# Optimization experiments

Measured on AMD Instinct MI355X. Metric: run time of the kernel, lower is better.

The kernel has to match this reference:

```python
import jax, jax.numpy as jnp
import numpy as np

EXP_CLAMP = 1.0e6
DENOM_EPS = 1e-10
LRELU_ALPHA = 0.01


def setup_inputs() -> dict:
    key = jax.random.key(0)
    k1, k2, k3, k4, k5, k6 = jax.random.split(key, 6)
    B, N, E, F = 4, 16384, 262144, 64
    h = jax.random.normal(k1, (B, N, F), dtype=jnp.float32)
    edge = jax.random.randint(k2, (B, E, 2), 0, N, dtype=jnp.int32)
    edge_num = jax.random.randint(k3, (B,), 1, E, dtype=jnp.int32)
    edge_weight = jax.random.uniform(k4, (B, E), dtype=jnp.float32)
    W = jax.random.normal(k5, (F, F), dtype=jnp.float32) * 0.15  # xavier-ish scale
    a = jax.random.normal(k6, (1, 2 * F), dtype=jnp.float32) * 0.12
    return {"h": h, "edge": edge, "edge_num": edge_num,
            "edge_weight": edge_weight, "W": W, "a": a}


def _seg_sum(src, idx, num_segments):
    # src: [E, ...], idx: [E] -> [num_segments, ...]
    return jax.ops.segment_sum(src, idx, num_segments=num_segments)


def reference(h, edge, edge_num, edge_weight, W, a):
    B, N, Fin = h.shape
    E = edge.shape[1]
    # linear transform: Wh = h @ W^T  -> [B, N, Fout]
    Wh = jnp.einsum('bnf,of->bno', h, W)
    ctr = edge[:, :, 0]  # [B, E]
    nbr = edge[:, :, 1]  # [B, E]
    Wh_c = jnp.take_along_axis(Wh, ctr[:, :, None], axis=1)  # [B, E, Fout]
    Wh_n = jnp.take_along_axis(Wh, nbr[:, :, None], axis=1)  # [B, E, Fout]
    a_input = jnp.concatenate([Wh_c, Wh_n], axis=-1) * edge_weight[:, :, None]
    # attention logits: leakyrelu(a_input @ a^T), squeeze to [B, E]
    att1 = jax.nn.leaky_relu(jnp.einsum('bek,k->be', a_input, a[0]), LRELU_ALPHA)
    # per-batch valid-edge mask (edges beyond edge_num zeroed, as in torch loop)
    mask = (jnp.arange(E, dtype=jnp.int32)[None, :] < edge_num[:, None])
    x_exp = jnp.clip(jnp.exp(att1), 0.0, EXP_CLAMP) * mask.astype(att1.dtype)
    # segment softmax denominator over center nodes
    denom = DENOM_EPS + jax.vmap(_seg_sum, in_axes=(0, 0, None))(x_exp, ctr, N)  # [B, N]
    att = x_exp / jnp.take_along_axis(denom, ctr, axis=1)  # [B, E]
    # weighted neighbor aggregation via scatter-add on center index
    att_Wh = Wh_n * att[:, :, None]  # masked edges already have att == 0
    h_prime = jax.vmap(_seg_sum, in_axes=(0, 0, None))(att_Wh, ctr, N)  # [B, N, Fout]
    return jax.nn.relu(h_prime)
```

## Files before the change

### kernel.cpp

```cpp
#include <hip/hip_runtime.h>

#define BB 4
#define NN 16384
#define EE 262144
#define FF 64
#define ROWS (BB * NN)
#define CAP 64

typedef __bf16 bf16x8 __attribute__((ext_vector_type(8)));
typedef float  f32x4  __attribute__((ext_vector_type(4)));

__device__ __forceinline__ unsigned short f32_to_bf16(float f) {
    unsigned int u = __float_as_uint(f);
    u += 0x7FFFu + ((u >> 16) & 1u);
    return (unsigned short)(u >> 16);
}

__global__ __launch_bounds__(256) void scsn_kernel(
    const float* __restrict__ h, const float* __restrict__ W,
    const float* __restrict__ a,
    float* __restrict__ sc, float* __restrict__ sn, int* __restrict__ cnt)
{
    __shared__ float wc[FF], wn[FF];
    const int t = threadIdx.x;

    if (blockIdx.x < 256) cnt[blockIdx.x * 256 + t] = 0;

    if (t < 128) {
        const int f = t & 63;
        const float* av = a + (t >> 6) * FF;
        float s = 0.0f;
        #pragma unroll 8
        for (int o = 0; o < FF; ++o)
            s = fmaf(av[o], W[o * FF + f], s);
        (t < 64 ? wc : wn)[f] = s;
    }
    __syncthreads();

    const int gl   = t & 15;
    const int rloc = t >> 4;
    const float4 wcv = *(const float4*)&wc[gl * 4];
    const float4 wnv = *(const float4*)&wn[gl * 4];

    for (int base = blockIdx.x * 16; base < ROWS; base += gridDim.x * 16) {
        const int row = base + rloc;
        const float4 hv = ((const float4*)h)[(size_t)row * 16 + gl];
        float s1 = hv.x * wcv.x + hv.y * wcv.y + hv.z * wcv.z + hv.w * wcv.w;
        float s2 = hv.x * wnv.x + hv.y * wnv.y + hv.z * wnv.z + hv.w * wnv.w;
        #pragma unroll
        for (int off = 8; off; off >>= 1) {
            s1 += __shfl_xor(s1, off);
            s2 += __shfl_xor(s2, off);
        }
        if (gl == 0) { sc[row] = s1; sn[row] = s2; }
    }
}

__global__ __launch_bounds__(256) void mfma_bin_kernel(
    const float* __restrict__ h, const float* __restrict__ W,
    const int* __restrict__ edge, const int* __restrict__ edge_num,
    const float* __restrict__ ew,
    const float* __restrict__ sc, const float* __restrict__ sn,
    unsigned short* __restrict__ Wh, int* __restrict__ cnt,
    unsigned int* __restrict__ payload)
{
    const int t = threadIdx.x;
    const int lane = t & 63;
    const int m = lane & 15;
    const int q = lane >> 4;

    bf16x8 bfrag[4][2];
    #pragma unroll
    for (int nt = 0; nt < 4; ++nt) {
        const float* wr = W + (nt * 16 + m) * FF;
        #pragma unroll
        for (int kh = 0; kh < 2; ++kh) {
            const float4 v0 = *(const float4*)(wr + kh * 32 + q * 8);
            const float4 v1 = *(const float4*)(wr + kh * 32 + q * 8 + 4);
            bf16x8 b;
            b[0] = (__bf16)v0.x; b[1] = (__bf16)v0.y;
            b[2] = (__bf16)v0.z; b[3] = (__bf16)v0.w;
            b[4] = (__bf16)v1.x; b[5] = (__bf16)v1.y;
            b[6] = (__bf16)v1.z; b[7] = (__bf16)v1.w;
            bfrag[nt][kh] = b;
        }
    }

    {
        const int waveId = (blockIdx.x * 256 + t) >> 6;
        const int R0 = waveId * 16;
        const float* hr = h + (size_t)(R0 + m) * FF;
        bf16x8 af[2];
        #pragma unroll
        for (int kh = 0; kh < 2; ++kh) {
            const float4 v0 = *(const float4*)(hr + kh * 32 + q * 8);
            const float4 v1 = *(const float4*)(hr + kh * 32 + q * 8 + 4);
            bf16x8 aa;
            aa[0] = (__bf16)v0.x; aa[1] = (__bf16)v0.y;
            aa[2] = (__bf16)v0.z; aa[3] = (__bf16)v0.w;
            aa[4] = (__bf16)v1.x; aa[5] = (__bf16)v1.y;
            aa[6] = (__bf16)v1.z; aa[7] = (__bf16)v1.w;
            af[kh] = aa;
        }
        #pragma unroll
        for (int nt = 0; nt < 4; ++nt) {
            f32x4 acc = {0.f, 0.f, 0.f, 0.f};
            acc = __builtin_amdgcn_mfma_f32_16x16x32_bf16(af[0], bfrag[nt][0], acc, 0, 0, 0);
            acc = __builtin_amdgcn_mfma_f32_16x16x32_bf16(af[1], bfrag[nt][1], acc, 0, 0, 0);
            #pragma unroll
            for (int i = 0; i < 4; ++i)
                Wh[(size_t)(R0 + q * 4 + i) * FF + nt * 16 + m] = f32_to_bf16(acc[i]);
        }
    }

    for (int i2 = blockIdx.x * 256 + t; i2 < (BB * EE) / 2;
         i2 += gridDim.x * 256) {
        const int b  = i2 >> 17;
        const int e0 = (2 * i2) & (EE - 1);
        const int en = edge_num[b];
        if (e0 >= en) continue;
        const int4   e4 = ((const int4*)edge)[i2];
        const float2 w2 = ((const float2*)ew)[i2];
        const int row0 = b * NN + e4.x;
        const int row1 = b * NN + e4.z;
        const bool act1 = (e0 + 1 < en);

        const int pos0 = atomicAdd(&cnt[row0], 1);
        const int pos1 = act1 ? atomicAdd(&cnt[row1], 1) : CAP;

        const float* snB = sn + b * NN;
        float att0 = w2.x * (sc[row0] + snB[e4.y]);
        att0 = att0 > 0.0f ? att0 : 0.01f * att0;
        const float xe0 = fminf(__expf(att0), 1000000.0f);
        unsigned int u0 = (__float_as_uint(xe0) + 0x2000u) & 0xFFFFC000u;
        if (pos0 < CAP)
            payload[(size_t)row0 * CAP + pos0] = u0 | (unsigned int)e4.y;

        if (act1) {
            float att1 = w2.y * (sc[row1] + snB[e4.w]);
            att1 = att1 > 0.0f ? att1 : 0.01f * att1;
            const float xe1 = fminf(__expf(att1), 1000000.0f);
            unsigned int u1 = (__float_as_uint(xe1) + 0x2000u) & 0xFFFFC000u;
            if (pos1 < CAP)
                payload[(size_t)row1 * CAP + pos1] = u1 | (unsigned int)e4.w;
        }
    }
}

__global__ __launch_bounds__(256) void gather_kernel(
    const int* __restrict__ cnt, const unsigned int* __restrict__ payload,
    const uint2* __restrict__ Wh2,
    float* __restrict__ out)
{
    const int bi = blockIdx.x;
    const int xcd = bi & 7;
    const int batch = xcd >> 1;
    const int within = ((bi >> 3) << 1) | (xcd & 1);
    const int rg = batch * 4096 + within;

    const int lane = threadIdx.x & 63;
    const int wave = threadIdx.x >> 6;
    const int row = rg * 4 + wave;
    const int grp = lane >> 4;
    const int gl  = lane & 15;
    int deg = cnt[row];
    if (deg > CAP) deg = CAP;
    const unsigned int* pl = payload + (size_t)row * CAP;
    const uint2* WhB = Wh2 + (size_t)batch * NN * 16;

    float a0 = 0.f, a1 = 0.f, a2 = 0.f, a3 = 0.f, dsum = 0.f;
    const unsigned int p = (lane < deg) ? pl[lane] : 0u;
    for (int jj = 0; jj < deg; jj += 16) {
        const unsigned int pv0 = __shfl(p, jj + grp);
        const unsigned int pv1 = __shfl(p, jj + grp + 4);
        const unsigned int pv2 = __shfl(p, jj + grp + 8);
        const unsigned int pv3 = __shfl(p, jj + grp + 12);
        const uint2 w0 = WhB[(size_t)(pv0 & 0x3FFFu) * 16 + gl];
        const uint2 w1 = WhB[(size_t)(pv1 & 0x3FFFu) * 16 + gl];
        const uint2 w2 = WhB[(size_t)(pv2 & 0x3FFFu) * 16 + gl];
        const uint2 w3 = WhB[(size_t)(pv3 & 0x3FFFu) * 16 + gl];
        const float xe0 = __uint_as_float(pv0 & 0xFFFFC000u);
        const float xe1 = __uint_as_float(pv1 & 0xFFFFC000u);
        const float xe2 = __uint_as_float(pv2 & 0xFFFFC000u);
        const float xe3 = __uint_as_float(pv3 & 0xFFFFC000u);
        a0 = fmaf(xe0, __uint_as_float(w0.x << 16),         a0);
        a1 = fmaf(xe0, __uint_as_float(w0.x & 0xFFFF0000u), a1);
        a2 = fmaf(xe0, __uint_as_float(w0.y << 16),         a2);
        a3 = fmaf(xe0, __uint_as_float(w0.y & 0xFFFF0000u), a3);
        a0 = fmaf(xe1, __uint_as_float(w1.x << 16),         a0);
        a1 = fmaf(xe1, __uint_as_float(w1.x & 0xFFFF0000u), a1);
        a2 = fmaf(xe1, __uint_as_float(w1.y << 16),         a2);
        a3 = fmaf(xe1, __uint_as_float(w1.y & 0xFFFF0000u), a3);
        a0 = fmaf(xe2, __uint_as_float(w2.x << 16),         a0);
        a1 = fmaf(xe2, __uint_as_float(w2.x & 0xFFFF0000u), a1);
        a2 = fmaf(xe2, __uint_as_float(w2.y << 16),         a2);
        a3 = fmaf(xe2, __uint_as_float(w2.y & 0xFFFF0000u), a3);
        a0 = fmaf(xe3, __uint_as_float(w3.x << 16),         a0);
        a1 = fmaf(xe3, __uint_as_float(w3.x & 0xFFFF0000u), a1);
        a2 = fmaf(xe3, __uint_as_float(w3.y << 16),         a2);
        a3 = fmaf(xe3, __uint_as_float(w3.y & 0xFFFF0000u), a3);
        dsum += (xe0 + xe1) + (xe2 + xe3);
    }
    a0 += __shfl_xor(a0, 16); a1 += __shfl_xor(a1, 16);
    a2 += __shfl_xor(a2, 16); a3 += __shfl_xor(a3, 16);
    dsum += __shfl_xor(dsum, 16);
    a0 += __shfl_xor(a0, 32); a1 += __shfl_xor(a1, 32);
    a2 += __shfl_xor(a2, 32); a3 += __shfl_xor(a3, 32);
    dsum += __shfl_xor(dsum, 32);

    if (grp == 0) {
        const float inv = 1.0f / (1e-10f + dsum);
        float4 o;
        o.x = fmaxf(a0 * inv, 0.0f);
        o.y = fmaxf(a1 * inv, 0.0f);
        o.z = fmaxf(a2 * inv, 0.0f);
        o.w = fmaxf(a3 * inv, 0.0f);
        ((float4*)out)[(size_t)row * 16 + gl] = o;
    }
}

extern "C" void kernel_launch(void* const* d_in, const int* in_sizes, int n_in,
                              void* d_out, int out_size, void* d_ws, size_t ws_size,
                              hipStream_t stream)
{
    const float* h        = (const float*)d_in[0];
    const int*   edge     = (const int*)  d_in[1];
    const int*   edge_num = (const int*)  d_in[2];
    const float* ew       = (const float*)d_in[3];
    const float* W        = (const float*)d_in[4];
    const float* a        = (const float*)d_in[5];
    float* out = (float*)d_out;

    unsigned short* Wh = (unsigned short*)d_ws;
    float* sc        = (float*)(Wh + (size_t)BB * NN * FF);
    float* sn        = sc + ROWS;
    int*   cnt       = (int*)(sn + ROWS);
    unsigned int* payload = (unsigned int*)(cnt + ROWS);

    scsn_kernel<<<1024, 256, 0, stream>>>(h, W, a, sc, sn, cnt);

    mfma_bin_kernel<<<1024, 256, 0, stream>>>(h, W, edge, edge_num, ew,
                                              sc, sn, Wh, cnt, payload);

    gather_kernel<<<ROWS / 4, 256, 0, stream>>>(cnt, payload,
                                                (const uint2*)Wh, out);
}
```

Before: 139.4 us.

## Fuse score projection into MFMA kernel and defer edge softmax logits to gather

```diff
diff --git a/kernel.cpp b/kernel.cpp
--- a/kernel.cpp
+++ b/kernel.cpp
@@ -16,15 +16,19 @@
     return (unsigned short)(u >> 16);
 }
 
-__global__ __launch_bounds__(256) void scsn_kernel(
+__global__ __launch_bounds__(256) void mfma_bin_kernel(
     const float* __restrict__ h, const float* __restrict__ W,
     const float* __restrict__ a,
-    float* __restrict__ sc, float* __restrict__ sn, int* __restrict__ cnt)
+    const int* __restrict__ edge, const int* __restrict__ edge_num,
+    unsigned short* __restrict__ Wh,
+    float* __restrict__ sc, float* __restrict__ sn,
+    int* __restrict__ cnt, unsigned int* __restrict__ payload)
 {
     __shared__ float wc[FF], wn[FF];
     const int t = threadIdx.x;
-
-    if (blockIdx.x < 256) cnt[blockIdx.x * 256 + t] = 0;
+    const int lane = t & 63;
+    const int m = lane & 15;
+    const int q = lane >> 4;
 
     if (t < 128) {
         const int f = t & 63;
@@ -35,39 +39,6 @@
             s = fmaf(av[o], W[o * FF + f], s);
         (t < 64 ? wc : wn)[f] = s;
     }
-    __syncthreads();
-
-    const int gl   = t & 15;
-    const int rloc = t >> 4;
-    const float4 wcv = *(const float4*)&wc[gl * 4];
-    const float4 wnv = *(const float4*)&wn[gl * 4];
-
-    for (int base = blockIdx.x * 16; base < ROWS; base += gridDim.x * 16) {
-        const int row = base + rloc;
-        const float4 hv = ((const float4*)h)[(size_t)row * 16 + gl];
-        float s1 = hv.x * wcv.x + hv.y * wcv.y + hv.z * wcv.z + hv.w * wcv.w;
-        float s2 = hv.x * wnv.x + hv.y * wnv.y + hv.z * wnv.z + hv.w * wnv.w;
-        #pragma unroll
-        for (int off = 8; off; off >>= 1) {
-            s1 += __shfl_xor(s1, off);
-            s2 += __shfl_xor(s2, off);
-        }
-        if (gl == 0) { sc[row] = s1; sn[row] = s2; }
-    }
-}
-
-__global__ __launch_bounds__(256) void mfma_bin_kernel(
-    const float* __restrict__ h, const float* __restrict__ W,
-    const int* __restrict__ edge, const int* __restrict__ edge_num,
-    const float* __restrict__ ew,
-    const float* __restrict__ sc, const float* __restrict__ sn,
-    unsigned short* __restrict__ Wh, int* __restrict__ cnt,
-    unsigned int* __restrict__ payload)
-{
-    const int t = threadIdx.x;
-    const int lane = t & 63;
-    const int m = lane & 15;
-    const int q = lane >> 4;
 
     bf16x8 bfrag[4][2];
     #pragma unroll
@@ -86,11 +57,14 @@
         }
     }
 
+    __syncthreads();
+
     {
         const int waveId = (blockIdx.x * 256 + t) >> 6;
         const int R0 = waveId * 16;
         const float* hr = h + (size_t)(R0 + m) * FF;
         bf16x8 af[2];
+        float s1 = 0.0f, s2 = 0.0f;
         #pragma unroll
         for (int kh = 0; kh < 2; ++kh) {
             const float4 v0 = *(const float4*)(hr + kh * 32 + q * 8);
@@ -101,7 +75,20 @@
             aa[4] = (__bf16)v1.x; aa[5] = (__bf16)v1.y;
             aa[6] = (__bf16)v1.z; aa[7] = (__bf16)v1.w;
             af[kh] = aa;
+            const int fb = kh * 32 + q * 8;
+            const float4 c0 = *(const float4*)&wc[fb];
+            const float4 c1 = *(const float4*)&wc[fb + 4];
+            const float4 n0 = *(const float4*)&wn[fb];
+            const float4 n1 = *(const float4*)&wn[fb + 4];
+            s1 = fmaf(v0.x, c0.x, fmaf(v0.y, c0.y, fmaf(v0.z, c0.z, fmaf(v0.w, c0.w, s1))));
+            s1 = fmaf(v1.x, c1.x, fmaf(v1.y, c1.y, fmaf(v1.z, c1.z, fmaf(v1.w, c1.w, s1))));
+            s2 = fmaf(v0.x, n0.x, fmaf(v0.y, n0.y, fmaf(v0.z, n0.z, fmaf(v0.w, n0.w, s2))));
+            s2 = fmaf(v1.x, n1.x, fmaf(v1.y, n1.y, fmaf(v1.z, n1.z, fmaf(v1.w, n1.w, s2))));
         }
+        s1 += __shfl_xor(s1, 16); s2 += __shfl_xor(s2, 16);
+        s1 += __shfl_xor(s1, 32); s2 += __shfl_xor(s2, 32);
+        if (lane < 16) { sc[R0 + m] = s1; sn[R0 + m] = s2; }
+
         #pragma unroll
         for (int nt = 0; nt < 4; ++nt) {
             f32x4 acc = {0.f, 0.f, 0.f, 0.f};
@@ -119,8 +106,7 @@
         const int e0 = (2 * i2) & (EE - 1);
         const int en = edge_num[b];
         if (e0 >= en) continue;
-        const int4   e4 = ((const int4*)edge)[i2];
-        const float2 w2 = ((const float2*)ew)[i2];
+        const int4 e4 = ((const int4*)edge)[i2];
         const int row0 = b * NN + e4.x;
         const int row1 = b * NN + e4.z;
         const bool act1 = (e0 + 1 < en);
@@ -128,28 +114,20 @@
         const int pos0 = atomicAdd(&cnt[row0], 1);
         const int pos1 = act1 ? atomicAdd(&cnt[row1], 1) : CAP;
 
-        const float* snB = sn + b * NN;
-        float att0 = w2.x * (sc[row0] + snB[e4.y]);
-        att0 = att0 > 0.0f ? att0 : 0.01f * att0;
-        const float xe0 = fminf(__expf(att0), 1000000.0f);
-        unsigned int u0 = (__float_as_uint(xe0) + 0x2000u) & 0xFFFFC000u;
         if (pos0 < CAP)
-            payload[(size_t)row0 * CAP + pos0] = u0 | (unsigned int)e4.y;
-
-        if (act1) {
-            float att1 = w2.y * (sc[row1] + snB[e4.w]);
-            att1 = att1 > 0.0f ? att1 : 0.01f * att1;
-            const float xe1 = fminf(__expf(att1), 1000000.0f);
-            unsigned int u1 = (__float_as_uint(xe1) + 0x2000u) & 0xFFFFC000u;
-            if (pos1 < CAP)
-                payload[(size_t)row1 * CAP + pos1] = u1 | (unsigned int)e4.w;
-        }
+            payload[(size_t)row0 * CAP + pos0] =
+                ((unsigned int)e0 << 14) | (unsigned int)e4.y;
+        if (act1 && pos1 < CAP)
+            payload[(size_t)row1 * CAP + pos1] =
+                ((unsigned int)(e0 + 1) << 14) | (unsigned int)e4.w;
     }
 }
 
 __global__ __launch_bounds__(256) void gather_kernel(
     const int* __restrict__ cnt, const unsigned int* __restrict__ payload,
     const uint2* __restrict__ Wh2,
+    const float* __restrict__ sc, const float* __restrict__ sn,
+    const float* __restrict__ ew,
     float* __restrict__ out)
 {
     const int bi = blockIdx.x;
@@ -167,9 +145,20 @@
     if (deg > CAP) deg = CAP;
     const unsigned int* pl = payload + (size_t)row * CAP;
     const uint2* WhB = Wh2 + (size_t)batch * NN * 16;
+    const float* snB = sn + batch * NN;
+    const float* ewB = ew + (size_t)batch * EE;
+    const float scr = sc[row];
+
+    unsigned int p = 0u;
+    if (lane < deg) {
+        const unsigned int raw = pl[lane];
+        const float s0 = ewB[raw >> 14] * (scr + snB[raw & 0x3FFFu]);
+        const float s1 = s0 > 0.0f ? s0 : 0.01f * s0;
+        const float xe = fminf(__expf(s1), 1000000.0f);
+        p = ((__float_as_uint(xe) + 0x2000u) & 0xFFFFC000u) | (raw & 0x3FFFu);
+    }
 
     float a0 = 0.f, a1 = 0.f, a2 = 0.f, a3 = 0.f, dsum = 0.f;
-    const unsigned int p = (lane < deg) ? pl[lane] : 0u;
     for (int jj = 0; jj < deg; jj += 16) {
         const unsigned int pv0 = __shfl(p, jj + grp);
         const unsigned int pv1 = __shfl(p, jj + grp + 4);
@@ -237,11 +226,12 @@
     int*   cnt       = (int*)(sn + ROWS);
     unsigned int* payload = (unsigned int*)(cnt + ROWS);
 
-    scsn_kernel<<<1024, 256, 0, stream>>>(h, W, a, sc, sn, cnt);
-
-    mfma_bin_kernel<<<1024, 256, 0, stream>>>(h, W, edge, edge_num, ew,
-                                              sc, sn, Wh, cnt, payload);
+    hipMemsetAsync(cnt, 0, ROWS * sizeof(int), stream);
+
+    mfma_bin_kernel<<<1024, 256, 0, stream>>>(h, W, a, edge, edge_num,
+                                              Wh, sc, sn, cnt, payload);
 
     gather_kernel<<<ROWS / 4, 256, 0, stream>>>(cnt, payload,
-                                                (const uint2*)Wh, out);
-}
+                                                (const uint2*)Wh,
+                                                sc, sn, ew, out);
+}
```

New measurement: 151.0 us. 1.08x slower.
